# Kernel optimization log

Measured on AMD Instinct MI355X. Metric: run time of the kernel, lower is better.

The kernel has to match this reference:

```python
import jax, jax.numpy as jnp
import numpy as np
import math

ALPHA = 1.0  # surrogate-gradient sharpness, self.alpha() == 1.0

@jax.custom_vjp
def spike(x):
    # Heaviside forward (PiecewiseQuadratic.apply forward)
    return (x >= 0).astype(x.dtype)

def _spike_fwd(x):
    return spike(x), x

def _spike_bwd(x, g):
    # piecewise-quadratic surrogate: g'(x) = alpha - alpha^2*|x| for |x| < 1/alpha, else 0
    sg = jnp.where(jnp.abs(x) < 1.0 / ALPHA, -(ALPHA ** 2) * jnp.abs(x) + ALPHA, 0.0)
    return (g * sg.astype(x.dtype),)

spike.defvjp(_spike_fwd, _spike_bwd)


def setup_inputs() -> dict:
    key = jax.random.key(0)
    kx = jax.random.fold_in(key, 0)
    B, T, N = 64, 64, 8192
    x = jax.random.normal(kx, (B, T, N), dtype=jnp.float32)
    # parameters per __init__: tau=2.0 -> stored param log(1/(tau-1)) = 0.0
    tau_p = jnp.array([math.log(1.0 / (2.0 - 1.0))], dtype=jnp.float32)
    lamb = jnp.array([0.2], dtype=jnp.float32)
    th = jnp.array([1.0], dtype=jnp.float32)  # non-learnable
    return {"x": x, "tau_p": tau_p, "lamb": lamb, "th": th}


def reference(x, tau_p, lamb, th):
    sig = jax.nn.sigmoid(tau_p)  # scalar leak factor, shape [1]
    xt = jnp.swapaxes(x, 0, 1)   # [T, B, N] for scan over time

    def step(last, x_t):
        u = last * sig + x_t
        s = spike(u - th)
        new_last = (u + lamb * (u - last)) * (1.0 - s)  # momentum + hard reset
        return new_last, s

    last0 = jnp.zeros_like(x[:, 0])
    _, out = jax.lax.scan(step, last0, xt)  # out: [T, B, N]
    return jnp.swapaxes(out, 0, 1)         # [B, T, N]
```

## Files before the change

### kernel.cpp

```cpp
#include <hip/hip_runtime.h>


#define LIF_B 64
#define LIF_T 64
#define LIF_N 8192
#define UN 8
#define NSTAGE (LIF_T / UN)

__global__ __launch_bounds__(256, 8) void lif_fwd_kernel(
    const float* __restrict__ x,
    const float* __restrict__ tau_p,
    const float* __restrict__ lamb_p,
    const float* __restrict__ th_p,
    float* __restrict__ out)
{
    const int tid = blockIdx.x * blockDim.x + threadIdx.x;
    const int b   = tid >> 13;
    const int n   = tid & (LIF_N - 1);

    const float sig  = 1.0f / (1.0f + expf(-tau_p[0]));
    const float lamb = lamb_p[0];
    const float th   = th_p[0];

    float last = 0.0f;
    const size_t base = (size_t)b * LIF_T * LIF_N + n;

    float cur[UN], nxt[UN];

#pragma unroll
    for (int i = 0; i < UN; ++i)
        cur[i] = x[base + (size_t)i * LIF_N];

#pragma unroll
    for (int k = 0; k < NSTAGE; ++k) {
        if (k + 1 < NSTAGE) {
#pragma unroll
            for (int i = 0; i < UN; ++i)
                nxt[i] = x[base + (size_t)((k + 1) * UN + i) * LIF_N];
        }

#pragma unroll
        for (int i = 0; i < UN; ++i) {
            float u = __fadd_rn(__fmul_rn(last, sig), cur[i]);
            float s = (u >= th) ? 1.0f : 0.0f;
            last = __fmul_rn(__fadd_rn(u, __fmul_rn(lamb, __fsub_rn(u, last))),
                             __fsub_rn(1.0f, s));
            __builtin_nontemporal_store(s, &out[base + (size_t)(k * UN + i) * LIF_N]);
        }

#pragma unroll
        for (int i = 0; i < UN; ++i)
            cur[i] = nxt[i];
    }
}

extern "C" void kernel_launch(void* const* d_in, const int* in_sizes, int n_in,
                              void* d_out, int out_size, void* d_ws, size_t ws_size,
                              hipStream_t stream) {
    (void)in_sizes; (void)n_in; (void)out_size; (void)d_ws; (void)ws_size;

    const float* x     = (const float*)d_in[0];
    const float* tau_p = (const float*)d_in[1];
    const float* lamb  = (const float*)d_in[2];
    const float* th    = (const float*)d_in[3];
    float*       out   = (float*)d_out;

    const int total_threads = LIF_B * LIF_N;
    const int block = 256;
    const int grid  = total_threads / block;

    lif_fwd_kernel<<<grid, block, 0, stream>>>(x, tau_p, lamb, th, out);
}
```

Before: 236.3 us.

## Vectorize LIF loads/stores to float4 with rolling deep prefetch pipeline

Each thread now handles two float4 groups of neurons and streams all 64 timesteps with a rolling 8-deep register prefetch buffer, using 128-bit loads and nontemporal stores. This cuts instruction count per byte and keeps more bytes in flight per thread. The grid shrinks eightfold, which lowers wave occupancy and may limit latency hiding.

```diff
diff --git a/kernel.cpp b/kernel.cpp
--- a/kernel.cpp
+++ b/kernel.cpp
@@ -4,53 +4,77 @@
 #define LIF_B 64
 #define LIF_T 64
 #define LIF_N 8192
-#define UN 8
-#define NSTAGE (LIF_T / UN)
+#define DPIPE 8
+#define CPT 2
 
-__global__ __launch_bounds__(256, 8) void lif_fwd_kernel(
+typedef float f4 __attribute__((ext_vector_type(4)));
+
+__global__ __launch_bounds__(256, 4) void lif_fwd_kernel(
     const float* __restrict__ x,
     const float* __restrict__ tau_p,
     const float* __restrict__ lamb_p,
     const float* __restrict__ th_p,
     float* __restrict__ out)
 {
-    const int tid = blockIdx.x * blockDim.x + threadIdx.x;
-    const int b   = tid >> 13;
-    const int n   = tid & (LIF_N - 1);
+    const int tid  = blockIdx.x * blockDim.x + threadIdx.x;
+    const int w    = tid >> 6;
+    const int lane = tid & 63;
+    const int b    = w >> 4;
+    const int n0   = ((w & 15) << 9) + (lane << 2);
 
     const float sig  = 1.0f / (1.0f + expf(-tau_p[0]));
     const float lamb = lamb_p[0];
     const float th   = th_p[0];
 
-    float last = 0.0f;
-    const size_t base = (size_t)b * LIF_T * LIF_N + n;
+    const size_t base = (size_t)b * (LIF_T * LIF_N) + n0;
 
-    float cur[UN], nxt[UN];
+    f4 buf[DPIPE][CPT];
+    float st[CPT][4];
+#pragma unroll
+    for (int c = 0; c < CPT; ++c)
+#pragma unroll
+        for (int e = 0; e < 4; ++e)
+            st[c][e] = 0.0f;
 
 #pragma unroll
-    for (int i = 0; i < UN; ++i)
-        cur[i] = x[base + (size_t)i * LIF_N];
+    for (int t = 0; t < DPIPE; ++t)
+#pragma unroll
+        for (int c = 0; c < CPT; ++c)
+            buf[t][c] = *(const f4*)(x + base + (size_t)t * LIF_N + c * 256);
 
 #pragma unroll
-    for (int k = 0; k < NSTAGE; ++k) {
-        if (k + 1 < NSTAGE) {
+    for (int t = 0; t < LIF_T; ++t) {
+        f4 cur[CPT];
 #pragma unroll
-            for (int i = 0; i < UN; ++i)
-                nxt[i] = x[base + (size_t)((k + 1) * UN + i) * LIF_N];
+        for (int c = 0; c < CPT; ++c)
+            cur[c] = buf[t & (DPIPE - 1)][c];
+
+        if (t + DPIPE < LIF_T) {
+#pragma unroll
+            for (int c = 0; c < CPT; ++c)
+                buf[t & (DPIPE - 1)][c] =
+                    *(const f4*)(x + base + (size_t)(t + DPIPE) * LIF_N + c * 256);
         }
 
 #pragma unroll
-        for (int i = 0; i < UN; ++i) {
-            float u = __fadd_rn(__fmul_rn(last, sig), cur[i]);
-            float s = (u >= th) ? 1.0f : 0.0f;
-            last = __fmul_rn(__fadd_rn(u, __fmul_rn(lamb, __fsub_rn(u, last))),
-                             __fsub_rn(1.0f, s));
-            __builtin_nontemporal_store(s, &out[base + (size_t)(k * UN + i) * LIF_N]);
+        for (int c = 0; c < CPT; ++c) {
+            f4 sv;
+#pragma unroll
+            for (int e = 0; e < 4; ++e) {
+                float last = st[c][e];
+                float xin  = (e == 0) ? cur[c].x : (e == 1) ? cur[c].y
+                           : (e == 2) ? cur[c].z : cur[c].w;
+                float u = __fadd_rn(__fmul_rn(last, sig), xin);
+                float s = (u >= th) ? 1.0f : 0.0f;
+                st[c][e] = __fmul_rn(
+                    __fadd_rn(u, __fmul_rn(lamb, __fsub_rn(u, last))),
+                    __fsub_rn(1.0f, s));
+                if (e == 0) sv.x = s; else if (e == 1) sv.y = s;
+                else if (e == 2) sv.z = s; else sv.w = s;
+            }
+            __builtin_nontemporal_store(sv,
+                (f4*)(out + base + (size_t)t * LIF_N + c * 256));
         }
-
-#pragma unroll
-        for (int i = 0; i < UN; ++i)
-            cur[i] = nxt[i];
     }
 }
 
@@ -65,7 +89,7 @@
     const float* th    = (const float*)d_in[3];
     float*       out   = (float*)d_out;
 
-    const int total_threads = LIF_B * LIF_N;
+    const int total_threads = LIF_B * LIF_N / (4 * CPT);
     const int block = 256;
     const int grid  = total_threads / block;
 
```

Result: no change. 238.4 us (+0.9%).
